# Performance work log

Hardware: AMD Instinct MI355X
Metric: run time of the kernel (lower is better)

## Reference

```python
import jax, jax.numpy as jnp
import numpy as np

D_MODEL = 512
NHEAD = 8
SEQ = 2048
BATCH = 4


def setup_inputs() -> dict:
    key = jax.random.key(0)
    ks = jax.random.split(key, 6)
    s = 0.02
    return {
        "x": jax.random.normal(ks[0], (SEQ, BATCH, D_MODEL), jnp.float32),
        "w_in_g": jax.random.normal(ks[1], (3 * D_MODEL, D_MODEL), jnp.float32) * s,
        "b_in_g": jnp.zeros((3 * D_MODEL,), jnp.float32),
        "w_out_g": jax.random.normal(ks[2], (D_MODEL, D_MODEL), jnp.float32) * s,
        "b_out_g": jnp.zeros((D_MODEL,), jnp.float32),
        "w_in_l": jax.random.normal(ks[3], (3 * D_MODEL, D_MODEL), jnp.float32) * s,
        "b_in_l": jnp.zeros((3 * D_MODEL,), jnp.float32),
        "w_out_l": jax.random.normal(ks[4], (D_MODEL, D_MODEL), jnp.float32) * s,
        "b_out_l": jnp.zeros((D_MODEL,), jnp.float32),
        "local_window_size": 128,
    }


def _mha(x, w_in, b_in, w_out, b_out, nhead):
    # x: (S, B, D); faithful to torch nn.MultiheadAttention (batch_first=False)
    S, B, D = x.shape
    dh = D // nhead
    qkv = x @ w_in.T + b_in                       # (S, B, 3D)
    q, k, v = jnp.split(qkv, 3, axis=-1)
    q = q.reshape(S, B, nhead, dh)
    k = k.reshape(S, B, nhead, dh)
    v = v.reshape(S, B, nhead, dh)
    scores = jnp.einsum("sbhd,tbhd->bhst", q, k) / jnp.sqrt(jnp.float32(dh))
    attn = jax.nn.softmax(scores, axis=-1)        # (B, H, S, S)
    out = jnp.einsum("bhst,tbhd->sbhd", attn, v).reshape(S, B, D)
    return out @ w_out.T + b_out


def reference(x, w_in_g, b_in_g, w_out_g, b_out_g,
              w_in_l, b_in_l, w_out_l, b_out_l, local_window_size):
    S, B, D = x.shape
    W = int(local_window_size)
    global_out = _mha(x, w_in_g, b_in_g, w_out_g, b_out_g, NHEAD)
    # Non-overlapping local windows tile the sequence (S % W == 0 here),
    # so the per-window loop == window-batched attention.
    nW = S // W
    xw = x.reshape(nW, W, B, D).transpose(1, 0, 2, 3).reshape(W, nW * B, D)
    lw = _mha(xw, w_in_l, b_in_l, w_out_l, b_out_l, NHEAD)
    local_out = lw.reshape(W, nW, B, D).transpose(1, 0, 2, 3).reshape(S, B, D)
    return global_out + local_out
```

## Files before the change

kernel.cpp:

```cpp
#include <hip/hip_runtime.h>
#include <hip/hip_bf16.h>
#include <stdint.h>

typedef __attribute__((ext_vector_type(8))) short bf16x8;
typedef __attribute__((ext_vector_type(4))) float f32x4;

#define DEV __device__ __forceinline__

DEV f32x4 mfma16(bf16x8 a, bf16x8 b, f32x4 c) {
  return __builtin_amdgcn_mfma_f32_16x16x32_bf16(a, b, c, 0, 0, 0);
}

DEV void gload_lds16(const void* g, void* l) {
  __builtin_amdgcn_global_load_lds(
      (__attribute__((address_space(1))) void*)(g),
      (__attribute__((address_space(3))) void*)(l), 16, 0, 0);
}

DEV unsigned short f2bf(float f) {
  __hip_bfloat16 h = __float2bfloat16(f);
  return __builtin_bit_cast(unsigned short, h);
}

__global__ __launch_bounds__(256) void convert_all(
    const float4* __restrict__ s0, const float4* __restrict__ s1,
    const float4* __restrict__ s2, const float4* __restrict__ s3,
    const float4* __restrict__ s4, ushort4* __restrict__ dst)
{
  const int n0 = 1048576, n1 = 196608, n3 = 65536;
  int i = blockIdx.x * 256 + threadIdx.x;
  const float4* s; int off;
  if (i < n0)                 { s = s0; off = 0; }
  else if (i < n0 + n1)       { s = s1; off = n0; }
  else if (i < n0 + 2*n1)     { s = s2; off = n0 + n1; }
  else if (i < n0 + 2*n1+n3)  { s = s3; off = n0 + 2*n1; }
  else                        { s = s4; off = n0 + 2*n1 + n3; }
  float4 v = s[i - off];
  ushort4 o;
  o.x = f2bf(v.x); o.y = f2bf(v.y); o.z = f2bf(v.z); o.w = f2bf(v.w);
  dst[i] = o;
}

__global__ __launch_bounds__(256) void gemm_qkv(
    const __hip_bfloat16* __restrict__ A0, const __hip_bfloat16* __restrict__ W0,
    const float* __restrict__ b0,
    __hip_bfloat16* __restrict__ qkp, __hip_bfloat16* __restrict__ vtp,
    int M, int N, int K)
{
  __shared__ __attribute__((aligned(16))) __hip_bfloat16 As[128*64];
  __shared__ __attribute__((aligned(16))) __hip_bfloat16 Ws[128*64];
  const int t = threadIdx.x;
  const int lane = t & 63, wid = t >> 6;
  const int wr = wid >> 1, wc = wid & 1;
  const int lid = blockIdx.x + (blockIdx.y << 6);
  const int xcd = lid & 7, pos = lid >> 3;
  const int m0 = (xcd*8 + (pos & 7)) * 128, n0 = (pos >> 3) * 128;

  f32x4 acc[4][4] = {};
  const int nks = K >> 6;

  for (int step = 0; step < nks; ++step) {
    const int k0 = step << 6;
#pragma unroll
    for (int is = 0; is < 4; ++is) {
      const int row = is*32 + (t >> 3);
      const int slot = (t & 7) ^ (row & 7);
      gload_lds16(A0 + (long)(m0 + row)*K + k0 + slot*8, (char*)As + (is*256 + t)*16);
      gload_lds16(W0 + (long)(n0 + row)*K + k0 + slot*8, (char*)Ws + (is*256 + t)*16);
    }
    __syncthreads();
#pragma unroll
    for (int kk = 0; kk < 2; ++kk) {
      bf16x8 af[4], wf[4];
#pragma unroll
      for (int i = 0; i < 4; ++i) {
        const int row = wr*64 + i*16 + (lane & 15);
        const int slot = (kk*4 + (lane >> 4)) ^ (row & 7);
        af[i] = *(const bf16x8*)((const char*)As + row*128 + slot*16);
      }
#pragma unroll
      for (int j = 0; j < 4; ++j) {
        const int row = wc*64 + j*16 + (lane & 15);
        const int slot = (kk*4 + (lane >> 4)) ^ (row & 7);
        wf[j] = *(const bf16x8*)((const char*)Ws + row*128 + slot*16);
      }
#pragma unroll
      for (int i = 0; i < 4; ++i)
#pragma unroll
        for (int j = 0; j < 4; ++j)
          acc[i][j] = mfma16(af[i], wf[j], acc[i][j]);
    }
    __syncthreads();
  }

#pragma unroll
  for (int i = 0; i < 4; ++i) {
    const int gr = m0 + wr*64 + i*16 + ((lane >> 4) << 2);
#pragma unroll
    for (int j = 0; j < 4; ++j) {
      const int gc = n0 + wc*64 + j*16 + (lane & 15);
      const float bias = b0[gc];
      if (gc < 1024) {
#pragma unroll
        for (int r = 0; r < 4; ++r)
          qkp[(long)(gr + r)*1024 + gc] = __float2bfloat16(acc[i][j][r] + bias);
      } else {
#pragma unroll
        for (int r = 0; r < 4; ++r) {
          const int m = gr + r;
          vtp[(long)((m & 3)*512 + gc - 1024)*2048 + (m >> 2)] =
              __float2bfloat16(acc[i][j][r] + bias);
        }
      }
    }
  }
}

__global__ __launch_bounds__(256) void gemm_out(
    const __hip_bfloat16* __restrict__ A0, const __hip_bfloat16* __restrict__ W0,
    const float* __restrict__ b0,
    const __hip_bfloat16* __restrict__ A1, const __hip_bfloat16* __restrict__ W1,
    const float* __restrict__ b1,
    float* __restrict__ Cout, int M, int N, int K)
{
  __shared__ __attribute__((aligned(16))) __hip_bfloat16 As[128*64];
  __shared__ __attribute__((aligned(16))) __hip_bfloat16 Ws[128*64];
  const int t = threadIdx.x;
  const int lane = t & 63, wid = t >> 6;
  const int wr = wid >> 1, wc = wid & 1;
  const int lid = blockIdx.x + (blockIdx.y << 6);
  const int xcd = lid & 7, pos = lid >> 3;
  const int m0 = (xcd*8 + (pos & 7)) * 128, n0 = (pos >> 3) * 128;

  f32x4 acc[4][4] = {};
  const int nks = K >> 6;

  for (int step = 0; step < 2*nks; ++step) {
    const int srcsel = step >= nks;
    const int k0 = (srcsel ? step - nks : step) << 6;
    const __hip_bfloat16* Ap = srcsel ? A1 : A0;
    const __hip_bfloat16* Wp = srcsel ? W1 : W0;
#pragma unroll
    for (int is = 0; is < 4; ++is) {
      const int row = is*32 + (t >> 3);
      const int slot = (t & 7) ^ (row & 7);
      gload_lds16(Ap + (long)(m0 + row)*K + k0 + slot*8, (char*)As + (is*256 + t)*16);
      gload_lds16(Wp + (long)(n0 + row)*K + k0 + slot*8, (char*)Ws + (is*256 + t)*16);
    }
    __syncthreads();
#pragma unroll
    for (int kk = 0; kk < 2; ++kk) {
      bf16x8 af[4], wf[4];
#pragma unroll
      for (int i = 0; i < 4; ++i) {
        const int row = wr*64 + i*16 + (lane & 15);
        const int slot = (kk*4 + (lane >> 4)) ^ (row & 7);
        af[i] = *(const bf16x8*)((const char*)As + row*128 + slot*16);
      }
#pragma unroll
      for (int j = 0; j < 4; ++j) {
        const int row = wc*64 + j*16 + (lane & 15);
        const int slot = (kk*4 + (lane >> 4)) ^ (row & 7);
        wf[j] = *(const bf16x8*)((const char*)Ws + row*128 + slot*16);
      }
#pragma unroll
      for (int i = 0; i < 4; ++i)
#pragma unroll
        for (int j = 0; j < 4; ++j)
          acc[i][j] = mfma16(af[i], wf[j], acc[i][j]);
    }
    __syncthreads();
  }

#pragma unroll
  for (int i = 0; i < 4; ++i) {
    const int gr = m0 + wr*64 + i*16 + ((lane >> 4) << 2);
#pragma unroll
    for (int j = 0; j < 4; ++j) {
      const int gc = n0 + wc*64 + j*16 + (lane & 15);
      const float bias = b0[gc] + b1[gc];
#pragma unroll
      for (int r = 0; r < 4; ++r)
        Cout[(long)(gr + r)*N + gc] = acc[i][j][r] + bias;
    }
  }
}

__global__ __launch_bounds__(512) void flash_all(
    const __hip_bfloat16* __restrict__ qkg, const __hip_bfloat16* __restrict__ vtg,
    __hip_bfloat16* __restrict__ outg,
    const __hip_bfloat16* __restrict__ qkl, const __hip_bfloat16* __restrict__ vtl,
    __hip_bfloat16* __restrict__ outl,
    const int* __restrict__ wptr, int S, int B, int blkoff)
{
  const int t = threadIdx.x, lane = t & 63, w = t >> 6;
  const int g16 = lane >> 4, l16 = lane & 15;
  const int gid = blockIdx.x + blkoff;
  const int isl = gid >= 512;
  const int id = gid & 511;
  const __hip_bfloat16* qk = isl ? qkl : qkg;
  const __hip_bfloat16* vt = isl ? vtl : vtg;
  __hip_bfloat16* outb = isl ? outl : outg;
  const int Wn = isl ? wptr[0] : S;
  const int xcd = id & 7, seq = id >> 3;
  const int bh = xcd + 8*(seq & 3);
  const int qt = seq >> 2;
  const int b = bh >> 3, h = bh & 7;
  const int q0 = qt * 128;
  const int kv0 = (q0 / Wn) * Wn;
  const int nkt = Wn >> 6;
  const int vtb = bh * 64;

  __shared__ __attribute__((aligned(16))) __hip_bfloat16 Kb[2][64*64];
  __shared__ __attribute__((aligned(16))) __hip_bfloat16 Vb[2][64*64];
  __shared__ __attribute__((aligned(16))) short Pl[8][16*72];

  const int qrow = q0 + w*16 + l16;
  bf16x8 qa[2];
  {
    const __hip_bfloat16* qp = qk + ((long)qrow*B + b)*1024 + h*64 + g16*8;
    qa[0] = *(const bf16x8*)(const void*)qp;
    qa[1] = *(const bf16x8*)(const void*)(qp + 32);
  }
  bf16x8 aones;
#pragma unroll
  for (int e = 0; e < 8; ++e) aones[e] = (short)0x3F80;

  f32x4 o[4] = {};
  f32x4 ol = {};
  const float c2 = 0.125f * 1.44269504088896f;

#define STAGE(tile, bufi)                                                      \
  {                                                                            \
    const int kvs_ = kv0 + (tile)*64;                                          \
    const int row_ = t >> 3;                                                   \
    const int sl_ = (t & 7) ^ (row_ & 7);                                      \
    gload_lds16(qk + ((long)(kvs_+row_)*B + b)*1024 + 512 + h*64 + sl_*8,      \
                (char*)&Kb[bufi][0] + t*16);                                   \
    gload_lds16(vt + (long)(vtb + row_)*2048 + kvs_ + sl_*8,                   \
                (char*)&Vb[bufi][0] + t*16);                                   \
  }

  STAGE(0, 0)

  for (int kt = 0; kt < nkt; ++kt) {
    const int cur = kt & 1;
    if (kt + 1 < nkt) {
      STAGE(kt + 1, cur ^ 1)
      asm volatile("s_waitcnt vmcnt(2)" ::: "memory");
    } else {
      asm volatile("s_waitcnt vmcnt(0)" ::: "memory");
    }
    __builtin_amdgcn_s_barrier();
    asm volatile("" ::: "memory");

    f32x4 s[4] = {};
    const char* Kp = (const char*)&Kb[cur][0];
    __builtin_amdgcn_s_setprio(1);
#pragma unroll
    for (int kk = 0; kk < 2; ++kk)
#pragma unroll
      for (int j = 0; j < 4; ++j) {
        const int row = j*16 + l16;
        const int slot = (kk*4 + g16) ^ (row & 7);
        bf16x8 kf = *(const bf16x8*)(Kp + row*128 + slot*16);
        s[j] = mfma16(kf, qa[kk], s[j]);
      }
    __builtin_amdgcn_s_setprio(0);

    short* Pw = &Pl[w][0];
#pragma unroll
    for (int j = 0; j < 4; ++j) {
      short4 pk4;
      pk4.x = (short)f2bf(__builtin_amdgcn_exp2f(s[j][0]*c2));
      pk4.y = (short)f2bf(__builtin_amdgcn_exp2f(s[j][1]*c2));
      pk4.z = (short)f2bf(__builtin_amdgcn_exp2f(s[j][2]*c2));
      pk4.w = (short)f2bf(__builtin_amdgcn_exp2f(s[j][3]*c2));
      *(short4*)(Pw + l16*72 + j*16 + g16*4) = pk4;
    }
    asm volatile("s_waitcnt lgkmcnt(0)" ::: "memory");
    __builtin_amdgcn_sched_barrier(0);

    __builtin_amdgcn_s_setprio(1);
#pragma unroll
    for (int kk = 0; kk < 2; ++kk) {
      bf16x8 pf = *(const bf16x8*)(Pw + l16*72 + kk*32 + g16*8);
      ol = mfma16(aones, pf, ol);
#pragma unroll
      for (int dblk = 0; dblk < 4; ++dblk) {
        const int row = dblk*16 + l16;
        const int slot = (kk*4 + g16) ^ (row & 7);
        bf16x8 vf = *(const bf16x8*)((const char*)&Vb[cur][0] + row*128 + slot*16);
        o[dblk] = mfma16(vf, pf, o[dblk]);
      }
    }
    __builtin_amdgcn_s_setprio(0);

    asm volatile("" ::: "memory");
    __builtin_amdgcn_s_barrier();
  }

  const float inv = 1.f / ol[0];
  const long obase = ((long)qrow*B + b)*512 + h*64;
#pragma unroll
  for (int dblk = 0; dblk < 4; ++dblk) {
    ushort4 pk;
    pk.x = f2bf(o[dblk][0]*inv); pk.y = f2bf(o[dblk][1]*inv);
    pk.z = f2bf(o[dblk][2]*inv); pk.w = f2bf(o[dblk][3]*inv);
    *(ushort4*)(outb + obase + dblk*16 + g16*4) = pk;
  }
}

extern "C" void kernel_launch(void* const* d_in, const int* in_sizes, int n_in,
                              void* d_out, int out_size, void* d_ws, size_t ws_size,
                              hipStream_t stream) {
  const float* x   = (const float*)d_in[0];
  const float* wig = (const float*)d_in[1];
  const float* big = (const float*)d_in[2];
  const float* wog = (const float*)d_in[3];
  const float* bog = (const float*)d_in[4];
  const float* wil = (const float*)d_in[5];
  const float* bil = (const float*)d_in[6];
  const float* wol = (const float*)d_in[7];
  const float* bol = (const float*)d_in[8];
  const int*   wsz = (const int*)d_in[9];

  char* ws = (char*)d_ws;
  __hip_bfloat16* xb    = (__hip_bfloat16*)(ws + 0);
  __hip_bfloat16* wigb  = (__hip_bfloat16*)(ws + 8388608);
  __hip_bfloat16* wilb  = (__hip_bfloat16*)(ws + 9961472);
  __hip_bfloat16* wogb  = (__hip_bfloat16*)(ws + 11534336);
  __hip_bfloat16* wolb  = (__hip_bfloat16*)(ws + 12058624);
  __hip_bfloat16* qkg   = (__hip_bfloat16*)(ws + 12582912);
  __hip_bfloat16* qkl   = (__hip_bfloat16*)(ws + 29360128);
  __hip_bfloat16* vtg   = (__hip_bfloat16*)(ws + 46137344);
  __hip_bfloat16* vtl   = (__hip_bfloat16*)(ws + 54525952);
  __hip_bfloat16* attng = xb;

  const int big_ws = ws_size >= (size_t)71303168;
  __hip_bfloat16* attnl = big_ws ? (__hip_bfloat16*)(ws + 62914560)
                                 : qkg;

  convert_all<<<6144, 256, 0, stream>>>(
      (const float4*)x, (const float4*)wig, (const float4*)wil,
      (const float4*)wog, (const float4*)wol, (ushort4*)ws);

  dim3 gq(64, 12);
  gemm_qkv<<<gq, 256, 0, stream>>>(xb, wigb, big, qkg, vtg, 8192, 1536, 512);
  gemm_qkv<<<gq, 256, 0, stream>>>(xb, wilb, bil, qkl, vtl, 8192, 1536, 512);

  if (big_ws) {
    flash_all<<<1024, 512, 0, stream>>>(qkg, vtg, attng, qkl, vtl, attnl,
                                        wsz, 2048, 4, 0);
  } else {
    flash_all<<<512, 512, 0, stream>>>(qkg, vtg, attng, qkl, vtl, attnl,
                                       wsz, 2048, 4, 0);
    flash_all<<<512, 512, 0, stream>>>(qkg, vtg, attng, qkl, vtl, attnl,
                                       wsz, 2048, 4, 512);
  }

  dim3 go(64, 4);
  gemm_out<<<go, 256, 0, stream>>>(attng, wogb, bog, attnl, wolb, bol,
                                   (float*)d_out, 8192, 512, 512);
}
```

Measured before the change: 133.7 us.

## Keep softmax P in registers and use K16 MFMA for PV with reordered V

Drops the per-warp LDS round trip for the probability tile. The exp'd scores now stay in registers as bf16x4 fragments and feed 16x16x16 MFMAs directly, and the V tile staging layout is reorganised to match that operand layout. This removes the LDS writes, the lgkmcnt wait and the re-reads of P. The cost is twice as many MFMA instructions for PV and the row sum, each with half the K depth, which may have lower throughput than the x32 variant. The V LDS layout also no longer uses the XOR swizzle, which could cause bank conflicts.

```diff
diff --git a/kernel.cpp b/kernel.cpp
--- a/kernel.cpp
+++ b/kernel.cpp
@@ -3,12 +3,29 @@
 #include <stdint.h>
 
 typedef __attribute__((ext_vector_type(8))) short bf16x8;
+typedef __attribute__((ext_vector_type(4))) short bf16x4;
 typedef __attribute__((ext_vector_type(4))) float f32x4;
 
 #define DEV __device__ __forceinline__
 
 DEV f32x4 mfma16(bf16x8 a, bf16x8 b, f32x4 c) {
   return __builtin_amdgcn_mfma_f32_16x16x32_bf16(a, b, c, 0, 0, 0);
+}
+
+DEV f32x4 mfma_k16(bf16x4 a, bf16x4 b, f32x4 c) {
+#if defined(__HIP_DEVICE_COMPILE__)
+#if __has_builtin(__builtin_amdgcn_mfma_f32_16x16x16bf16_1k)
+  return __builtin_amdgcn_mfma_f32_16x16x16bf16_1k(a, b, c, 0, 0, 0);
+#else
+  f32x4 d;
+  asm volatile("v_mfma_f32_16x16x16_bf16 %0, %1, %2, %3"
+               : "=v"(d) : "v"(a), "v"(b), "v"(c));
+  return d;
+#endif
+#else
+  (void)a; (void)b;
+  return c;
+#endif
 }
 
 DEV void gload_lds16(const void* g, void* l) {
@@ -213,7 +230,6 @@
 
   __shared__ __attribute__((aligned(16))) __hip_bfloat16 Kb[2][64*64];
   __shared__ __attribute__((aligned(16))) __hip_bfloat16 Vb[2][64*64];
-  __shared__ __attribute__((aligned(16))) short Pl[8][16*72];
 
   const int qrow = q0 + w*16 + l16;
   bf16x8 qa[2];
@@ -222,9 +238,9 @@
     qa[0] = *(const bf16x8*)(const void*)qp;
     qa[1] = *(const bf16x8*)(const void*)(qp + 32);
   }
-  bf16x8 aones;
-#pragma unroll
-  for (int e = 0; e < 8; ++e) aones[e] = (short)0x3F80;
+  bf16x4 ones4;
+#pragma unroll
+  for (int e = 0; e < 4; ++e) ones4[e] = (short)0x3F80;
 
   f32x4 o[4] = {};
   f32x4 ol = {};
@@ -237,7 +253,8 @@
     const int sl_ = (t & 7) ^ (row_ & 7);                                      \
     gload_lds16(qk + ((long)(kvs_+row_)*B + b)*1024 + 512 + h*64 + sl_*8,      \
                 (char*)&Kb[bufi][0] + t*16);                                   \
-    gload_lds16(vt + (long)(vtb + row_)*2048 + kvs_ + sl_*8,                   \
+    const int vj_ = t >> 7, vd_ = (t >> 1) & 63, vh_ = t & 1;                  \
+    gload_lds16(vt + (long)(vtb + vd_)*2048 + kvs_ + vj_*16 + vh_*8,           \
                 (char*)&Vb[bufi][0] + t*16);                                   \
   }
 
@@ -268,30 +285,25 @@
       }
     __builtin_amdgcn_s_setprio(0);
 
-    short* Pw = &Pl[w][0];
+    bf16x4 pb[4];
 #pragma unroll
     for (int j = 0; j < 4; ++j) {
-      short4 pk4;
-      pk4.x = (short)f2bf(__builtin_amdgcn_exp2f(s[j][0]*c2));
-      pk4.y = (short)f2bf(__builtin_amdgcn_exp2f(s[j][1]*c2));
-      pk4.z = (short)f2bf(__builtin_amdgcn_exp2f(s[j][2]*c2));
-      pk4.w = (short)f2bf(__builtin_amdgcn_exp2f(s[j][3]*c2));
-      *(short4*)(Pw + l16*72 + j*16 + g16*4) = pk4;
-    }
-    asm volatile("s_waitcnt lgkmcnt(0)" ::: "memory");
-    __builtin_amdgcn_sched_barrier(0);
-
+      pb[j][0] = (short)f2bf(__builtin_amdgcn_exp2f(s[j][0]*c2));
+      pb[j][1] = (short)f2bf(__builtin_amdgcn_exp2f(s[j][1]*c2));
+      pb[j][2] = (short)f2bf(__builtin_amdgcn_exp2f(s[j][2]*c2));
+      pb[j][3] = (short)f2bf(__builtin_amdgcn_exp2f(s[j][3]*c2));
+    }
+
+    const char* Vp = (const char*)&Vb[cur][0];
     __builtin_amdgcn_s_setprio(1);
 #pragma unroll
-    for (int kk = 0; kk < 2; ++kk) {
-      bf16x8 pf = *(const bf16x8*)(Pw + l16*72 + kk*32 + g16*8);
-      ol = mfma16(aones, pf, ol);
+    for (int j = 0; j < 4; ++j) {
+      ol = mfma_k16(ones4, pb[j], ol);
 #pragma unroll
       for (int dblk = 0; dblk < 4; ++dblk) {
         const int row = dblk*16 + l16;
-        const int slot = (kk*4 + g16) ^ (row & 7);
-        bf16x8 vf = *(const bf16x8*)((const char*)&Vb[cur][0] + row*128 + slot*16);
-        o[dblk] = mfma16(vf, pf, o[dblk]);
+        bf16x4 va = *(const bf16x4*)(Vp + j*2048 + row*32 + g16*8);
+        o[dblk] = mfma_k16(va, pb[j], o[dblk]);
       }
     }
     __builtin_amdgcn_s_setprio(0);
```

Result: slower. 163.3 us (+22.1%).

## Double-buffer GEMM LDS tiles with 8-wave blocks and relax flash LDS wait

Applied to the files above, without the earlier changes.

Both projection GEMMs now prefetch the next k-tile into a second LDS buffer while computing the current one, synchronising through vmcnt waits and raw barriers. Blocks grow to 512 threads, with each wave owning a 64x32 output subtile, and MFMA sections run at raised priority. The flash kernel drops an explicit lgkmcnt wait and scheduling barrier between the P store and its reload. The aim is to hide global load latency and add wave-level parallelism, at the cost of doubled LDS per block and reliance on the compiler for the P read-after-write ordering.

```diff
diff --git a/kernel.cpp b/kernel.cpp
--- a/kernel.cpp
+++ b/kernel.cpp
@@ -41,64 +41,89 @@
   dst[i] = o;
 }
 
-__global__ __launch_bounds__(256) void gemm_qkv(
+#define GEMM_STAGE(Ap, Wp, k0v, bufi)                                          \
+  {                                                                            \
+    _Pragma("unroll")                                                          \
+    for (int is = 0; is < 2; ++is) {                                           \
+      const int row = is*64 + (t >> 3);                                        \
+      const int slot = (t & 7) ^ (row & 7);                                    \
+      gload_lds16((Ap) + (long)(m0 + row)*K + (k0v) + slot*8,                  \
+                  (char*)&As[bufi][0] + (is*512 + t)*16);                      \
+      gload_lds16((Wp) + (long)(n0 + row)*K + (k0v) + slot*8,                  \
+                  (char*)&Ws[bufi][0] + (is*512 + t)*16);                      \
+    }                                                                          \
+  }
+
+#define GEMM_COMPUTE(cur)                                                      \
+  {                                                                            \
+    const char* Apl = (const char*)&As[cur][0];                                \
+    const char* Wpl = (const char*)&Ws[cur][0];                                \
+    __builtin_amdgcn_s_setprio(1);                                             \
+    _Pragma("unroll")                                                          \
+    for (int kk = 0; kk < 2; ++kk) {                                           \
+      bf16x8 af[4], wf[2];                                                     \
+      _Pragma("unroll")                                                        \
+      for (int i = 0; i < 4; ++i) {                                            \
+        const int row = wr*64 + i*16 + l16;                                    \
+        const int slot = (kk*4 + g16) ^ (row & 7);                             \
+        af[i] = *(const bf16x8*)(Apl + row*128 + slot*16);                     \
+      }                                                                        \
+      _Pragma("unroll")                                                        \
+      for (int j = 0; j < 2; ++j) {                                            \
+        const int row = wc*32 + j*16 + l16;                                    \
+        const int slot = (kk*4 + g16) ^ (row & 7);                             \
+        wf[j] = *(const bf16x8*)(Wpl + row*128 + slot*16);                     \
+      }                                                                        \
+      _Pragma("unroll")                                                        \
+      for (int i = 0; i < 4; ++i)                                              \
+        _Pragma("unroll")                                                      \
+        for (int j = 0; j < 2; ++j)                                            \
+          acc[i][j] = mfma16(af[i], wf[j], acc[i][j]);                         \
+    }                                                                          \
+    __builtin_amdgcn_s_setprio(0);                                             \
+  }
+
+__global__ __launch_bounds__(512) void gemm_qkv(
     const __hip_bfloat16* __restrict__ A0, const __hip_bfloat16* __restrict__ W0,
     const float* __restrict__ b0,
     __hip_bfloat16* __restrict__ qkp, __hip_bfloat16* __restrict__ vtp,
     int M, int N, int K)
 {
-  __shared__ __attribute__((aligned(16))) __hip_bfloat16 As[128*64];
-  __shared__ __attribute__((aligned(16))) __hip_bfloat16 Ws[128*64];
+  __shared__ __attribute__((aligned(16))) __hip_bfloat16 As[2][128*64];
+  __shared__ __attribute__((aligned(16))) __hip_bfloat16 Ws[2][128*64];
   const int t = threadIdx.x;
   const int lane = t & 63, wid = t >> 6;
-  const int wr = wid >> 1, wc = wid & 1;
+  const int g16 = lane >> 4, l16 = lane & 15;
+  const int wr = wid >> 2, wc = wid & 3;
   const int lid = blockIdx.x + (blockIdx.y << 6);
   const int xcd = lid & 7, pos = lid >> 3;
   const int m0 = (xcd*8 + (pos & 7)) * 128, n0 = (pos >> 3) * 128;
 
-  f32x4 acc[4][4] = {};
+  f32x4 acc[4][2] = {};
   const int nks = K >> 6;
 
+  GEMM_STAGE(A0, W0, 0, 0)
   for (int step = 0; step < nks; ++step) {
-    const int k0 = step << 6;
-#pragma unroll
-    for (int is = 0; is < 4; ++is) {
-      const int row = is*32 + (t >> 3);
-      const int slot = (t & 7) ^ (row & 7);
-      gload_lds16(A0 + (long)(m0 + row)*K + k0 + slot*8, (char*)As + (is*256 + t)*16);
-      gload_lds16(W0 + (long)(n0 + row)*K + k0 + slot*8, (char*)Ws + (is*256 + t)*16);
-    }
-    __syncthreads();
-#pragma unroll
-    for (int kk = 0; kk < 2; ++kk) {
-      bf16x8 af[4], wf[4];
-#pragma unroll
-      for (int i = 0; i < 4; ++i) {
-        const int row = wr*64 + i*16 + (lane & 15);
-        const int slot = (kk*4 + (lane >> 4)) ^ (row & 7);
-        af[i] = *(const bf16x8*)((const char*)As + row*128 + slot*16);
-      }
-#pragma unroll
-      for (int j = 0; j < 4; ++j) {
-        const int row = wc*64 + j*16 + (lane & 15);
-        const int slot = (kk*4 + (lane >> 4)) ^ (row & 7);
-        wf[j] = *(const bf16x8*)((const char*)Ws + row*128 + slot*16);
-      }
-#pragma unroll
-      for (int i = 0; i < 4; ++i)
-#pragma unroll
-        for (int j = 0; j < 4; ++j)
-          acc[i][j] = mfma16(af[i], wf[j], acc[i][j]);
-    }
-    __syncthreads();
+    const int cur = step & 1;
+    if (step + 1 < nks) {
+      GEMM_STAGE(A0, W0, (step+1) << 6, cur ^ 1)
+      asm volatile("s_waitcnt vmcnt(4)" ::: "memory");
+    } else {
+      asm volatile("s_waitcnt vmcnt(0)" ::: "memory");
+    }
+    __builtin_amdgcn_s_barrier();
+    asm volatile("" ::: "memory");
+    GEMM_COMPUTE(cur)
+    asm volatile("" ::: "memory");
+    __builtin_amdgcn_s_barrier();
   }
 
 #pragma unroll
   for (int i = 0; i < 4; ++i) {
-    const int gr = m0 + wr*64 + i*16 + ((lane >> 4) << 2);
-#pragma unroll
-    for (int j = 0; j < 4; ++j) {
-      const int gc = n0 + wc*64 + j*16 + (lane & 15);
+    const int gr = m0 + wr*64 + i*16 + g16*4;
+#pragma unroll
+    for (int j = 0; j < 2; ++j) {
+      const int gc = n0 + wc*32 + j*16 + l16;
       const float bias = b0[gc];
       if (gc < 1024) {
 #pragma unroll
@@ -116,68 +141,53 @@
   }
 }
 
-__global__ __launch_bounds__(256) void gemm_out(
+__global__ __launch_bounds__(512) void gemm_out(
     const __hip_bfloat16* __restrict__ A0, const __hip_bfloat16* __restrict__ W0,
     const float* __restrict__ b0,
     const __hip_bfloat16* __restrict__ A1, const __hip_bfloat16* __restrict__ W1,
     const float* __restrict__ b1,
     float* __restrict__ Cout, int M, int N, int K)
 {
-  __shared__ __attribute__((aligned(16))) __hip_bfloat16 As[128*64];
-  __shared__ __attribute__((aligned(16))) __hip_bfloat16 Ws[128*64];
+  __shared__ __attribute__((aligned(16))) __hip_bfloat16 As[2][128*64];
+  __shared__ __attribute__((aligned(16))) __hip_bfloat16 Ws[2][128*64];
   const int t = threadIdx.x;
   const int lane = t & 63, wid = t >> 6;
-  const int wr = wid >> 1, wc = wid & 1;
+  const int g16 = lane >> 4, l16 = lane & 15;
+  const int wr = wid >> 2, wc = wid & 3;
   const int lid = blockIdx.x + (blockIdx.y << 6);
   const int xcd = lid & 7, pos = lid >> 3;
   const int m0 = (xcd*8 + (pos & 7)) * 128, n0 = (pos >> 3) * 128;
 
-  f32x4 acc[4][4] = {};
+  f32x4 acc[4][2] = {};
   const int nks = K >> 6;
-
-  for (int step = 0; step < 2*nks; ++step) {
-    const int srcsel = step >= nks;
-    const int k0 = (srcsel ? step - nks : step) << 6;
-    const __hip_bfloat16* Ap = srcsel ? A1 : A0;
-    const __hip_bfloat16* Wp = srcsel ? W1 : W0;
-#pragma unroll
-    for (int is = 0; is < 4; ++is) {
-      const int row = is*32 + (t >> 3);
-      const int slot = (t & 7) ^ (row & 7);
-      gload_lds16(Ap + (long)(m0 + row)*K + k0 + slot*8, (char*)As + (is*256 + t)*16);
-      gload_lds16(Wp + (long)(n0 + row)*K + k0 + slot*8, (char*)Ws + (is*256 + t)*16);
-    }
-    __syncthreads();
-#pragma unroll
-    for (int kk = 0; kk < 2; ++kk) {
-      bf16x8 af[4], wf[4];
-#pragma unroll
-      for (int i = 0; i < 4; ++i) {
-        const int row = wr*64 + i*16 + (lane & 15);
-        const int slot = (kk*4 + (lane >> 4)) ^ (row & 7);
-        af[i] = *(const bf16x8*)((const char*)As + row*128 + slot*16);
-      }
-#pragma unroll
-      for (int j = 0; j < 4; ++j) {
-        const int row = wc*64 + j*16 + (lane & 15);
-        const int slot = (kk*4 + (lane >> 4)) ^ (row & 7);
-        wf[j] = *(const bf16x8*)((const char*)Ws + row*128 + slot*16);
-      }
-#pragma unroll
-      for (int i = 0; i < 4; ++i)
-#pragma unroll
-        for (int j = 0; j < 4; ++j)
-          acc[i][j] = mfma16(af[i], wf[j], acc[i][j]);
-    }
-    __syncthreads();
+  const int NS = 2*nks;
+
+  GEMM_STAGE(A0, W0, 0, 0)
+  for (int step = 0; step < NS; ++step) {
+    const int cur = step & 1;
+    if (step + 1 < NS) {
+      const int nstep = step + 1;
+      const __hip_bfloat16* Ap = (nstep >= nks) ? A1 : A0;
+      const __hip_bfloat16* Wp = (nstep >= nks) ? W1 : W0;
+      const int k0 = ((nstep >= nks) ? (nstep - nks) : nstep) << 6;
+      GEMM_STAGE(Ap, Wp, k0, cur ^ 1)
+      asm volatile("s_waitcnt vmcnt(4)" ::: "memory");
+    } else {
+      asm volatile("s_waitcnt vmcnt(0)" ::: "memory");
+    }
+    __builtin_amdgcn_s_barrier();
+    asm volatile("" ::: "memory");
+    GEMM_COMPUTE(cur)
+    asm volatile("" ::: "memory");
+    __builtin_amdgcn_s_barrier();
   }
 
 #pragma unroll
   for (int i = 0; i < 4; ++i) {
-    const int gr = m0 + wr*64 + i*16 + ((lane >> 4) << 2);
-#pragma unroll
-    for (int j = 0; j < 4; ++j) {
-      const int gc = n0 + wc*64 + j*16 + (lane & 15);
+    const int gr = m0 + wr*64 + i*16 + g16*4;
+#pragma unroll
+    for (int j = 0; j < 2; ++j) {
+      const int gc = n0 + wc*32 + j*16 + l16;
       const float bias = b0[gc] + b1[gc];
 #pragma unroll
       for (int r = 0; r < 4; ++r)
@@ -278,8 +288,6 @@
       pk4.w = (short)f2bf(__builtin_amdgcn_exp2f(s[j][3]*c2));
       *(short4*)(Pw + l16*72 + j*16 + g16*4) = pk4;
     }
-    asm volatile("s_waitcnt lgkmcnt(0)" ::: "memory");
-    __builtin_amdgcn_sched_barrier(0);
 
     __builtin_amdgcn_s_setprio(1);
 #pragma unroll
@@ -346,8 +354,8 @@
       (const float4*)wog, (const float4*)wol, (ushort4*)ws);
 
   dim3 gq(64, 12);
-  gemm_qkv<<<gq, 256, 0, stream>>>(xb, wigb, big, qkg, vtg, 8192, 1536, 512);
-  gemm_qkv<<<gq, 256, 0, stream>>>(xb, wilb, bil, qkl, vtl, 8192, 1536, 512);
+  gemm_qkv<<<gq, 512, 0, stream>>>(xb, wigb, big, qkg, vtg, 8192, 1536, 512);
+  gemm_qkv<<<gq, 512, 0, stream>>>(xb, wilb, bil, qkl, vtl, 8192, 1536, 512);
 
   if (big_ws) {
     flash_all<<<1024, 512, 0, stream>>>(qkg, vtg, attng, qkl, vtl, attnl,
@@ -360,6 +368,6 @@
   }
 
   dim3 go(64, 4);
-  gemm_out<<<go, 256, 0, stream>>>(attng, wogb, bog, attnl, wolb, bol,
+  gemm_out<<<go, 512, 0, stream>>>(attng, wogb, bog, attnl, wolb, bol,
                                    (float*)d_out, 8192, 512, 512);
 }
```

Measured after the change: 132.6 us. About the same (-0.8%).
